# Optimization experiments

Hardware: AMD Instinct MI355X
Metric: run time of the kernel (lower is better)

The kernel has to match this reference:

```python
import jax, jax.numpy as jnp
import numpy as np

N, E, D, H, O = 50000, 600000, 128, 128, 64


def _glorot(key, shape):
    fan_in, fan_out = shape[-1], shape[0]
    lim = (6.0 / (fan_in + fan_out)) ** 0.5
    return jax.random.uniform(key, shape, jnp.float32, -lim, lim)


def setup_inputs() -> dict:
    key = jax.random.key(0)
    ks = jax.random.split(key, 20)
    inp = {
        'x': jax.random.normal(ks[0], (N, D), dtype=jnp.float32),
        'edge_index': jax.random.randint(ks[1], (2, E), 0, N, dtype=jnp.int32),
        # FastLocalConv params
        'fl_W': _glorot(ks[2], (H, D)),
        'fl_b': jnp.zeros((H,), jnp.float32),
        'fl_att': _glorot(ks[3], (1, H)),
        # GIN layer 1 MLP: Linear(H,H) -> ReLU -> Linear(H,H)
        'g1_W1': _glorot(ks[4], (H, H)), 'g1_b1': jnp.zeros((H,), jnp.float32),
        'g1_W2': _glorot(ks[5], (H, H)), 'g1_b2': jnp.zeros((H,), jnp.float32),
        # GIN layer 2 MLP
        'g2_W1': _glorot(ks[6], (H, H)), 'g2_b1': jnp.zeros((H,), jnp.float32),
        'g2_W2': _glorot(ks[7], (H, H)), 'g2_b2': jnp.zeros((H,), jnp.float32),
        # output head
        'out_W': _glorot(ks[8], (O, H)), 'out_b': jnp.zeros((O,), jnp.float32),
    }
    return inp


def _fast_local(x, edge_index, W, b, att):
    # add self loops
    loops = jnp.arange(N, dtype=edge_index.dtype)
    row = jnp.concatenate([edge_index[0], loops])
    col = jnp.concatenate([edge_index[1], loops])
    h = x @ W.T + b                                   # [N,H]
    alpha = jax.nn.leaky_relu((h[row] * att[0]).sum(-1), 0.2)  # [E+N]
    # scatter-softmax grouped by source node (row), as in original code
    m = jax.ops.segment_max(alpha, row, num_segments=N)
    ea = jnp.exp(alpha - m[row])
    s = jax.ops.segment_sum(ea, row, num_segments=N)
    a = ea / s[row]
    # aggr='add' into target nodes (col), message = alpha * x_j (x_j = h[row])
    return jax.ops.segment_sum(a[:, None] * h[row], col, num_segments=N)


def _gin(h, edge_index, W1, b1, W2, b2):
    # GINConv (eps=0): mlp(x + sum_{j in N(i)} x_j), no self loops
    agg = jax.ops.segment_sum(h[edge_index[0]], edge_index[1], num_segments=N)
    z = h + agg
    z = jax.nn.relu(z @ W1.T + b1)
    return z @ W2.T + b2


def reference(x, edge_index, fl_W, fl_b, fl_att,
              g1_W1, g1_b1, g1_W2, g1_b2,
              g2_W1, g2_b1, g2_W2, g2_b2,
              out_W, out_b):
    h = _fast_local(x, edge_index, fl_W, fl_b, fl_att)
    h = jax.nn.relu(h)  # (dropout is eval no-op)
    h = jax.nn.relu(_gin(h, edge_index, g1_W1, g1_b1, g1_W2, g1_b2))
    h = jax.nn.relu(_gin(h, edge_index, g2_W1, g2_b1, g2_W2, g2_b2))
    logits = h @ out_W.T + out_b
    return jax.nn.log_softmax(logits, axis=1)
```

## Files before the change

### kernel.cpp

```cpp
#include <hip/hip_runtime.h>
#include <stdint.h>

typedef __attribute__((ext_vector_type(8))) short short8;
typedef __attribute__((ext_vector_type(4))) float floatx4;

#define HB 64
#define HW 12500

__device__ inline unsigned short f2bf(float f) {
  union { float f; unsigned int u; } v; v.f = f;
  unsigned int u = v.u;
  unsigned int r = (u + 0x7FFFu + ((u >> 16) & 1u)) >> 16;
  return (unsigned short)r;
}
__device__ inline unsigned int pk2(float a, float b) {
  return (unsigned int)f2bf(a) | ((unsigned int)f2bf(b) << 16);
}
__device__ inline void acc8(uint4 u, float* a) {
  a[0] += __uint_as_float(u.x << 16); a[1] += __uint_as_float(u.x & 0xffff0000u);
  a[2] += __uint_as_float(u.y << 16); a[3] += __uint_as_float(u.y & 0xffff0000u);
  a[4] += __uint_as_float(u.z << 16); a[5] += __uint_as_float(u.z & 0xffff0000u);
  a[6] += __uint_as_float(u.w << 16); a[7] += __uint_as_float(u.w & 0xffff0000u);
}
__device__ inline uint4 pk8(const float* a) {
  uint4 p;
  p.x = pk2(a[0], a[1]); p.y = pk2(a[2], a[3]);
  p.z = pk2(a[4], a[5]); p.w = pk2(a[6], a[7]);
  return p;
}

__global__ __launch_bounds__(256) void k_wconv(const float* __restrict__ s0, const float* __restrict__ s1,
                                               const float* __restrict__ s2, const float* __restrict__ s3,
                                               const float* __restrict__ s4, const float* __restrict__ s5,
                                               unsigned short* __restrict__ dst) {
  int b = blockIdx.x;
  int seg = b >> 4;
  int rel = b & 15;
  const float* sp[6] = {s0, s1, s2, s3, s4, s5};
  const float* src = sp[seg];
  int i = rel * 1024 + threadIdx.x * 4;
  float4 v = *(const float4*)(src + i);
  size_t o = (size_t)seg * 16384 + i;
  *(uint2*)(dst + o) = make_uint2(pk2(v.x, v.y), pk2(v.z, v.w));
}

__global__ __launch_bounds__(1024) void k_hist(const int* __restrict__ esrc,
                                               const int* __restrict__ edst,
                                               int E, int per,
                                               unsigned int* __restrict__ pAll) {
  __shared__ unsigned int h[HW];
  for (int i = threadIdx.x; i < HW; i += 1024) h[i] = 0;
  __syncthreads();
  const int* idx = blockIdx.y ? esrc : edst;
  int s = blockIdx.x * per, e = min(E, s + per);
  for (int j = s + threadIdx.x; j < e; j += 1024) {
    unsigned int d = (unsigned int)idx[j];
    atomicAdd(&h[d >> 2], 1u << ((d & 3) * 8));
  }
  __syncthreads();
  unsigned int* p = pAll + ((size_t)blockIdx.y * HB + blockIdx.x) * HW;
  for (int i = threadIdx.x; i < HW; i += 1024) p[i] = h[i];
}

__global__ __launch_bounds__(256) void k_reduce(unsigned int* __restrict__ pAll,
                                                int* __restrict__ deg,
                                                float* __restrict__ invc, int N) {
  int w = blockIdx.x * 256 + threadIdx.x;
  if (w >= HW) return;
  unsigned int* pd = pAll + w;
  const unsigned int* ps = pAll + (size_t)HB * HW + w;
  unsigned int r0 = 0, r1 = 0, r2 = 0, r3 = 0;
  for (int b = 0; b < HB; ++b) {
    unsigned int v = pd[(size_t)b * HW];
    pd[(size_t)b * HW] = r0 | (r1 << 8) | (r2 << 16) | (r3 << 24);
    r0 += v & 255u; r1 += (v >> 8) & 255u; r2 += (v >> 16) & 255u; r3 += v >> 24;
  }
  unsigned int s0 = 0, s1 = 0, s2 = 0, s3 = 0;
  for (int b = 0; b < HB; ++b) {
    unsigned int v = ps[(size_t)b * HW];
    s0 += v & 255u; s1 += (v >> 8) & 255u; s2 += (v >> 16) & 255u; s3 += v >> 24;
  }
  int n0 = 4 * w;
  unsigned int rr[4] = {r0, r1, r2, r3}, ss[4] = {s0, s1, s2, s3};
#pragma unroll
  for (int c = 0; c < 4; ++c) {
    if (n0 + c < N) {
      deg[n0 + c] = (int)rr[c];
      invc[n0 + c] = 1.0f / (1.0f + (float)ss[c]);
    }
  }
}

__global__ __launch_bounds__(1024) void k_scan_local(const int* __restrict__ deg,
                                                     int* __restrict__ off,
                                                     int* __restrict__ bsum, int N) {
  __shared__ int sb[1024];
  int tid = threadIdx.x;
  int i = blockIdx.x * 1024 + tid;
  int v = (i < N) ? deg[i] : 0;
  sb[tid] = v;
  __syncthreads();
  for (int d = 1; d < 1024; d <<= 1) {
    int t = (tid >= d) ? sb[tid - d] : 0;
    __syncthreads();
    sb[tid] += t;
    __syncthreads();
  }
  if (i < N) off[i] = sb[tid] - v;
  if (tid == 1023) bsum[blockIdx.x] = sb[1023];
}

__global__ __launch_bounds__(256) void k_scan_fix(int* off, const int* __restrict__ bsum,
                                                  int N, int E) {
  int i = blockIdx.x * 256 + threadIdx.x;
  if (i >= N) return;
  int nb = i >> 10;
  int s = 0;
  for (int c = 0; c < nb; ++c) s += bsum[c];
  off[i] += s;
  if (i == 0) off[N] = E;
}

__global__ __launch_bounds__(1024) void k_fill2(const int* __restrict__ esrc,
                                                const int* __restrict__ edst,
                                                int E, int per,
                                                const unsigned int* __restrict__ pAll,
                                                const int* __restrict__ off,
                                                int* __restrict__ srcs) {
  __shared__ unsigned int rk[HW];
  for (int i = threadIdx.x; i < HW; i += 1024) rk[i] = 0;
  __syncthreads();
  const unsigned int* slab = pAll + (size_t)blockIdx.x * HW;
  int s = blockIdx.x * per, e = min(E, s + per);
  for (int j = s + threadIdx.x; j < e; j += 1024) {
    unsigned int d = (unsigned int)edst[j];
    int sh = (d & 3) * 8;
    unsigned int rank = (atomicAdd(&rk[d >> 2], 1u << sh) >> sh) & 255u;
    unsigned int base = (slab[d >> 2] >> sh) & 255u;
    srcs[off[d] + (int)base + (int)rank] = esrc[j];
  }
}

__global__ __launch_bounds__(256) void k_gemm_fl(const float* __restrict__ in,
                                                 const unsigned short* __restrict__ Wb,
                                                 const float* __restrict__ bias,
                                                 const float* __restrict__ scale,
                                                 unsigned short* __restrict__ out, int N) {
  __shared__ unsigned short sx[64 * 136];
  __shared__ unsigned short sw[128 * 136];
  const int tid = threadIdx.x;
  const int nb = blockIdx.x * 64;

  for (int i = tid; i < 128 * 16; i += 256) {
    int h = i >> 4, c = i & 15;
    *(short8*)&sw[h * 136 + c * 8] = ((const short8*)Wb)[i];
  }
  for (int i = tid; i < 64 * 32; i += 256) {
    int n = i >> 5, k4 = i & 31;
    int gn = nb + n;
    float4 xv;
    if (gn < N) xv = ((const float4*)in)[(size_t)gn * 32 + k4];
    else { xv.x = 0.f; xv.y = 0.f; xv.z = 0.f; xv.w = 0.f; }
    *(uint2*)&sx[n * 136 + k4 * 4] = make_uint2(pk2(xv.x, xv.y), pk2(xv.z, xv.w));
  }
  __syncthreads();

  const int wave = tid >> 6, lane = tid & 63;
  const int quad = lane >> 4, lq = lane & 15;
  floatx4 acc[8];
#pragma unroll
  for (int t = 0; t < 8; ++t) acc[t] = (floatx4){0.f, 0.f, 0.f, 0.f};
  const int arow = (wave * 16 + lq) * 136;
#pragma unroll
  for (int kt = 0; kt < 4; ++kt) {
    short8 a = *(const short8*)&sx[arow + kt * 32 + quad * 8];
#pragma unroll
    for (int t = 0; t < 8; ++t) {
      short8 b = *(const short8*)&sw[(t * 16 + lq) * 136 + kt * 32 + quad * 8];
      acc[t] = __builtin_amdgcn_mfma_f32_16x16x32_bf16(a, b, acc[t], 0, 0, 0);
    }
  }
#pragma unroll
  for (int t = 0; t < 8; ++t) {
    int h = t * 16 + lq;
    float bv = bias[h];
#pragma unroll
    for (int r = 0; r < 4; ++r) {
      int n = nb + wave * 16 + quad * 4 + r;
      if (n < N) out[(size_t)n * 128 + h] = f2bf((acc[t][r] + bv) * scale[n]);
    }
  }
}

template <bool RELU_OUT>
__global__ __launch_bounds__(256) void k_agg(const uint4* __restrict__ G,
                                             uint4* __restrict__ out,
                                             const int* __restrict__ off,
                                             const int* __restrict__ srcs, int N) {
  int n = (blockIdx.x * 256 + threadIdx.x) >> 4;
  if (n >= N) return;
  int l = threadIdx.x & 15;
  float a[8] = {0, 0, 0, 0, 0, 0, 0, 0};
  acc8(G[(size_t)n * 16 + l], a);
  int s = off[n], e = off[n + 1];
  int j = s;
  for (; j + 8 <= e; j += 8) {
    int i0 = srcs[j],     i1 = srcs[j + 1], i2 = srcs[j + 2], i3 = srcs[j + 3];
    int i4 = srcs[j + 4], i5 = srcs[j + 5], i6 = srcs[j + 6], i7 = srcs[j + 7];
    uint4 u0 = G[(size_t)i0 * 16 + l];
    uint4 u1 = G[(size_t)i1 * 16 + l];
    uint4 u2 = G[(size_t)i2 * 16 + l];
    uint4 u3 = G[(size_t)i3 * 16 + l];
    uint4 u4 = G[(size_t)i4 * 16 + l];
    uint4 u5 = G[(size_t)i5 * 16 + l];
    uint4 u6 = G[(size_t)i6 * 16 + l];
    uint4 u7 = G[(size_t)i7 * 16 + l];
    acc8(u0, a); acc8(u1, a); acc8(u2, a); acc8(u3, a);
    acc8(u4, a); acc8(u5, a); acc8(u6, a); acc8(u7, a);
  }
  if (j + 4 <= e) {
    int i0 = srcs[j], i1 = srcs[j + 1], i2 = srcs[j + 2], i3 = srcs[j + 3];
    uint4 u0 = G[(size_t)i0 * 16 + l];
    uint4 u1 = G[(size_t)i1 * 16 + l];
    uint4 u2 = G[(size_t)i2 * 16 + l];
    uint4 u3 = G[(size_t)i3 * 16 + l];
    acc8(u0, a); acc8(u1, a); acc8(u2, a); acc8(u3, a);
    j += 4;
  }
  for (; j < e; ++j) acc8(G[(size_t)srcs[j] * 16 + l], a);
  if (RELU_OUT) {
#pragma unroll
    for (int q = 0; q < 8; ++q) a[q] = fmaxf(a[q], 0.f);
  }
  out[(size_t)n * 16 + l] = pk8(a);
}

__global__ __launch_bounds__(256) void k_mlp(const unsigned short* __restrict__ in,
                                             const unsigned short* __restrict__ W1b,
                                             const float* __restrict__ b1,
                                             const unsigned short* __restrict__ W2b,
                                             const float* __restrict__ b2,
                                             unsigned short* __restrict__ out, int N) {
  __shared__ unsigned short sx[64 * 136];
  __shared__ unsigned short sw[128 * 136];
  const int tid = threadIdx.x;
  const int nb = blockIdx.x * 64;

  for (int i = tid; i < 128 * 16; i += 256) {
    int h = i >> 4, c = i & 15;
    *(short8*)&sw[h * 136 + c * 8] = ((const short8*)W1b)[i];
  }
  for (int i = tid; i < 64 * 16; i += 256) {
    int n = i >> 4, c = i & 15;
    int gn = nb + n;
    short8 t;
    if (gn < N) t = *(const short8*)(in + (size_t)gn * 128 + c * 8);
    else t = (short8){0, 0, 0, 0, 0, 0, 0, 0};
    *(short8*)&sx[n * 136 + c * 8] = t;
  }
  __syncthreads();

  const int wave = tid >> 6, lane = tid & 63;
  const int quad = lane >> 4, lq = lane & 15;
  const int arow = (wave * 16 + lq) * 136;

  floatx4 acc[8];
#pragma unroll
  for (int t = 0; t < 8; ++t) acc[t] = (floatx4){0.f, 0.f, 0.f, 0.f};
#pragma unroll
  for (int kt = 0; kt < 4; ++kt) {
    short8 a = *(const short8*)&sx[arow + kt * 32 + quad * 8];
#pragma unroll
    for (int t = 0; t < 8; ++t) {
      short8 b = *(const short8*)&sw[(t * 16 + lq) * 136 + kt * 32 + quad * 8];
      acc[t] = __builtin_amdgcn_mfma_f32_16x16x32_bf16(a, b, acc[t], 0, 0, 0);
    }
  }
  __syncthreads();

#pragma unroll
  for (int t = 0; t < 8; ++t) {
    int h = t * 16 + lq;
    float bv = b1[h];
#pragma unroll
    for (int r = 0; r < 4; ++r) {
      int row = wave * 16 + quad * 4 + r;
      sx[row * 136 + h] = f2bf(fmaxf(acc[t][r] + bv, 0.f));
    }
  }
  for (int i = tid; i < 128 * 16; i += 256) {
    int h = i >> 4, c = i & 15;
    *(short8*)&sw[h * 136 + c * 8] = ((const short8*)W2b)[i];
  }
  __syncthreads();

#pragma unroll
  for (int t = 0; t < 8; ++t) acc[t] = (floatx4){0.f, 0.f, 0.f, 0.f};
#pragma unroll
  for (int kt = 0; kt < 4; ++kt) {
    short8 a = *(const short8*)&sx[arow + kt * 32 + quad * 8];
#pragma unroll
    for (int t = 0; t < 8; ++t) {
      short8 b = *(const short8*)&sw[(t * 16 + lq) * 136 + kt * 32 + quad * 8];
      acc[t] = __builtin_amdgcn_mfma_f32_16x16x32_bf16(a, b, acc[t], 0, 0, 0);
    }
  }
#pragma unroll
  for (int t = 0; t < 8; ++t) {
    int h = t * 16 + lq;
    float bv = b2[h];
#pragma unroll
    for (int r = 0; r < 4; ++r) {
      int n = nb + wave * 16 + quad * 4 + r;
      if (n < N) out[(size_t)n * 128 + h] = f2bf(fmaxf(acc[t][r] + bv, 0.f));
    }
  }
}

__global__ __launch_bounds__(256) void k_head(const unsigned short* __restrict__ in,
                                              const unsigned short* __restrict__ Wb,
                                              const float* __restrict__ bias,
                                              float* __restrict__ out, int N) {
  __shared__ unsigned short sx[64 * 136];
  __shared__ unsigned short sw[64 * 136];
  const int tid = threadIdx.x;
  const int nb = blockIdx.x * 64;

  for (int i = tid; i < 64 * 16; i += 256) {
    int h = i >> 4, c = i & 15;
    *(short8*)&sw[h * 136 + c * 8] = ((const short8*)Wb)[i];
  }
  for (int i = tid; i < 64 * 16; i += 256) {
    int n = i >> 4, c = i & 15;
    int gn = nb + n;
    short8 t;
    if (gn < N) t = *(const short8*)(in + (size_t)gn * 128 + c * 8);
    else t = (short8){0, 0, 0, 0, 0, 0, 0, 0};
    *(short8*)&sx[n * 136 + c * 8] = t;
  }
  __syncthreads();

  const int wave = tid >> 6, lane = tid & 63;
  const int quad = lane >> 4, lq = lane & 15;
  floatx4 acc[4];
#pragma unroll
  for (int t = 0; t < 4; ++t) acc[t] = (floatx4){0.f, 0.f, 0.f, 0.f};
  const int arow = (wave * 16 + lq) * 136;
#pragma unroll
  for (int kt = 0; kt < 4; ++kt) {
    short8 a = *(const short8*)&sx[arow + kt * 32 + quad * 8];
#pragma unroll
    for (int t = 0; t < 4; ++t) {
      short8 b = *(const short8*)&sw[(t * 16 + lq) * 136 + kt * 32 + quad * 8];
      acc[t] = __builtin_amdgcn_mfma_f32_16x16x32_bf16(a, b, acc[t], 0, 0, 0);
    }
  }
  float v[4][4];
#pragma unroll
  for (int t = 0; t < 4; ++t) {
    float bv = bias[t * 16 + lq];
#pragma unroll
    for (int r = 0; r < 4; ++r) v[t][r] = acc[t][r] + bv;
  }
#pragma unroll
  for (int r = 0; r < 4; ++r) {
    float m = fmaxf(fmaxf(v[0][r], v[1][r]), fmaxf(v[2][r], v[3][r]));
    m = fmaxf(m, __shfl_xor(m, 1));
    m = fmaxf(m, __shfl_xor(m, 2));
    m = fmaxf(m, __shfl_xor(m, 4));
    m = fmaxf(m, __shfl_xor(m, 8));
    float s = expf(v[0][r] - m) + expf(v[1][r] - m) + expf(v[2][r] - m) + expf(v[3][r] - m);
    s += __shfl_xor(s, 1);
    s += __shfl_xor(s, 2);
    s += __shfl_xor(s, 4);
    s += __shfl_xor(s, 8);
    float l = m + logf(s);
    int n = nb + wave * 16 + quad * 4 + r;
    if (n < N) {
#pragma unroll
      for (int t = 0; t < 4; ++t) out[(size_t)n * 64 + t * 16 + lq] = v[t][r] - l;
    }
  }
}

extern "C" void kernel_launch(void* const* d_in, const int* in_sizes, int n_in,
                              void* d_out, int out_size, void* d_ws, size_t ws_size,
                              hipStream_t stream) {
  const float* x     = (const float*)d_in[0];
  const int*   edges = (const int*)  d_in[1];
  const float* fl_W  = (const float*)d_in[2];
  const float* fl_b  = (const float*)d_in[3];
  const float* g1_W1 = (const float*)d_in[5];
  const float* g1_b1 = (const float*)d_in[6];
  const float* g1_W2 = (const float*)d_in[7];
  const float* g1_b2 = (const float*)d_in[8];
  const float* g2_W1 = (const float*)d_in[9];
  const float* g2_b1 = (const float*)d_in[10];
  const float* g2_W2 = (const float*)d_in[11];
  const float* g2_b2 = (const float*)d_in[12];
  const float* out_W = (const float*)d_in[13];
  const float* out_b = (const float*)d_in[14];

  const int N = in_sizes[0] / 128;
  const int E = in_sizes[1] / 2;
  const int* esrc = edges;
  const int* edst = edges + E;

  char* w = (char*)d_ws;
  unsigned short* A = (unsigned short*)w;  w += (size_t)N * 128 * 2;
  unsigned short* B = (unsigned short*)w;  w += (size_t)N * 128 * 2;
  unsigned short* C = (unsigned short*)w;  w += (size_t)N * 128 * 2;
  unsigned short* Wb = (unsigned short*)w; w += 90112 * 2;
  int* deg    = (int*)w;   w += (size_t)N * 4;
  int* off    = (int*)w;   w += (size_t)(N + 1) * 4;
  float* invc = (float*)w; w += (size_t)N * 4;
  int* bsum   = (int*)w;   w += 1024 * 4;
  int* srcs   = (int*)w;   w += (size_t)E * 4;
  unsigned int* pAll = (unsigned int*)w; w += (size_t)2 * HB * HW * 4;

  const int GB = (N + 63) / 64;
  const int AGB = (N * 16 + 255) / 256;
  const int nchunk = (N + 1023) / 1024;
  const int per = (E + HB - 1) / HB;

  k_wconv<<<88, 256, 0, stream>>>(fl_W, g1_W1, g1_W2, g2_W1, g2_W2, out_W, Wb);

  k_hist<<<dim3(HB, 2), 1024, 0, stream>>>(esrc, edst, E, per, pAll);
  k_reduce<<<(HW + 255) / 256, 256, 0, stream>>>(pAll, deg, invc, N);
  k_scan_local<<<nchunk, 1024, 0, stream>>>(deg, off, bsum, N);
  k_scan_fix<<<(N + 255) / 256, 256, 0, stream>>>(off, bsum, N, E);
  k_fill2<<<HB, 1024, 0, stream>>>(esrc, edst, E, per, pAll, off, srcs);

  k_gemm_fl<<<GB, 256, 0, stream>>>(x, Wb, fl_b, invc, A, N);
  k_agg<true><<<AGB, 256, 0, stream>>>((const uint4*)A, (uint4*)B, off, srcs, N);

  k_agg<false><<<AGB, 256, 0, stream>>>((const uint4*)B, (uint4*)C, off, srcs, N);
  k_mlp<<<GB, 256, 0, stream>>>(C, Wb + 16384, g1_b1, Wb + 32768, g1_b2, A, N);

  k_agg<false><<<AGB, 256, 0, stream>>>((const uint4*)A, (uint4*)C, off, srcs, N);
  k_mlp<<<GB, 256, 0, stream>>>(C, Wb + 49152, g2_b1, Wb + 65536, g2_b2, B, N);

  k_head<<<GB, 256, 0, stream>>>(B, Wb + 81920, out_b, (float*)d_out, N);
}
```

Before: 295.8 us.

## Fuse degree reduction with local prefix scan and vectorize shared-memory clears

Merges the histogram reduction kernel and the local scan kernel into one kernel. Each thread handles four packed node counters and scans their sum, which removes the intermediate degree array and one launch. Each scan block now covers 4096 nodes, and the offsets are written as int4. Shared histogram zeroing and the copy-out now use uint4 accesses. The trade-off is that the fused kernel runs with only 13 blocks of 1024 threads, so the strided 64-slab reduction loop has little parallelism.

```diff
diff --git a/kernel.cpp b/kernel.cpp
--- a/kernel.cpp
+++ b/kernel.cpp
@@ -48,8 +48,9 @@
                                                const int* __restrict__ edst,
                                                int E, int per,
                                                unsigned int* __restrict__ pAll) {
-  __shared__ unsigned int h[HW];
-  for (int i = threadIdx.x; i < HW; i += 1024) h[i] = 0;
+  __shared__ __align__(16) unsigned int h[HW];
+  uint4* h4 = (uint4*)h;
+  for (int i = threadIdx.x; i < HW / 4; i += 1024) h4[i] = make_uint4(0, 0, 0, 0);
   __syncthreads();
   const int* idx = blockIdx.y ? esrc : edst;
   int s = blockIdx.x * per, e = min(E, s + per);
@@ -58,47 +59,45 @@
     atomicAdd(&h[d >> 2], 1u << ((d & 3) * 8));
   }
   __syncthreads();
-  unsigned int* p = pAll + ((size_t)blockIdx.y * HB + blockIdx.x) * HW;
-  for (int i = threadIdx.x; i < HW; i += 1024) p[i] = h[i];
-}
-
-__global__ __launch_bounds__(256) void k_reduce(unsigned int* __restrict__ pAll,
-                                                int* __restrict__ deg,
-                                                float* __restrict__ invc, int N) {
-  int w = blockIdx.x * 256 + threadIdx.x;
-  if (w >= HW) return;
-  unsigned int* pd = pAll + w;
-  const unsigned int* ps = pAll + (size_t)HB * HW + w;
-  unsigned int r0 = 0, r1 = 0, r2 = 0, r3 = 0;
-  for (int b = 0; b < HB; ++b) {
-    unsigned int v = pd[(size_t)b * HW];
-    pd[(size_t)b * HW] = r0 | (r1 << 8) | (r2 << 16) | (r3 << 24);
-    r0 += v & 255u; r1 += (v >> 8) & 255u; r2 += (v >> 16) & 255u; r3 += v >> 24;
-  }
-  unsigned int s0 = 0, s1 = 0, s2 = 0, s3 = 0;
-  for (int b = 0; b < HB; ++b) {
-    unsigned int v = ps[(size_t)b * HW];
-    s0 += v & 255u; s1 += (v >> 8) & 255u; s2 += (v >> 16) & 255u; s3 += v >> 24;
-  }
-  int n0 = 4 * w;
-  unsigned int rr[4] = {r0, r1, r2, r3}, ss[4] = {s0, s1, s2, s3};
-#pragma unroll
-  for (int c = 0; c < 4; ++c) {
-    if (n0 + c < N) {
-      deg[n0 + c] = (int)rr[c];
-      invc[n0 + c] = 1.0f / (1.0f + (float)ss[c]);
-    }
-  }
-}
-
-__global__ __launch_bounds__(1024) void k_scan_local(const int* __restrict__ deg,
-                                                     int* __restrict__ off,
-                                                     int* __restrict__ bsum, int N) {
+  uint4* p4 = (uint4*)(pAll + ((size_t)blockIdx.y * HB + blockIdx.x) * HW);
+  for (int i = threadIdx.x; i < HW / 4; i += 1024) p4[i] = h4[i];
+}
+
+__global__ __launch_bounds__(1024) void k_degscan(unsigned int* __restrict__ pAll,
+                                                  int* __restrict__ off,
+                                                  float* __restrict__ invc,
+                                                  int* __restrict__ bsum, int N) {
   __shared__ int sb[1024];
   int tid = threadIdx.x;
-  int i = blockIdx.x * 1024 + tid;
-  int v = (i < N) ? deg[i] : 0;
-  sb[tid] = v;
+  int w = blockIdx.x * 1024 + tid;
+  unsigned int r0 = 0, r1 = 0, r2 = 0, r3 = 0;
+  if (w < HW) {
+    unsigned int* pd = pAll + w;
+    for (int b = 0; b < HB; ++b) {
+      unsigned int v = pd[(size_t)b * HW];
+      pd[(size_t)b * HW] = r0 | (r1 << 8) | (r2 << 16) | (r3 << 24);
+      r0 += v & 255u; r1 += (v >> 8) & 255u; r2 += (v >> 16) & 255u; r3 += v >> 24;
+    }
+    const unsigned int* ps = pAll + (size_t)HB * HW + w;
+    unsigned int s0 = 0, s1 = 0, s2 = 0, s3 = 0;
+    for (int b = 0; b < HB; ++b) {
+      unsigned int v = ps[(size_t)b * HW];
+      s0 += v & 255u; s1 += (v >> 8) & 255u; s2 += (v >> 16) & 255u; s3 += v >> 24;
+    }
+    int n0 = 4 * w;
+    float i0 = 1.0f / (1.0f + (float)s0), i1 = 1.0f / (1.0f + (float)s1);
+    float i2 = 1.0f / (1.0f + (float)s2), i3 = 1.0f / (1.0f + (float)s3);
+    if (n0 + 3 < N) {
+      invc[n0] = i0; invc[n0 + 1] = i1; invc[n0 + 2] = i2; invc[n0 + 3] = i3;
+    } else {
+      if (n0 < N) invc[n0] = i0;
+      if (n0 + 1 < N) invc[n0 + 1] = i1;
+      if (n0 + 2 < N) invc[n0 + 2] = i2;
+      if (n0 + 3 < N) invc[n0 + 3] = i3;
+    }
+  }
+  int L = (w < HW) ? (int)(r0 + r1 + r2 + r3) : 0;
+  sb[tid] = L;
   __syncthreads();
   for (int d = 1; d < 1024; d <<= 1) {
     int t = (tid >= d) ? sb[tid - d] : 0;
@@ -106,7 +105,15 @@
     sb[tid] += t;
     __syncthreads();
   }
-  if (i < N) off[i] = sb[tid] - v;
+  int base = sb[tid] - L;
+  if (w < HW) {
+    int4 o;
+    o.x = base;
+    o.y = o.x + (int)r0;
+    o.z = o.y + (int)r1;
+    o.w = o.z + (int)r2;
+    *(int4*)(off + 4 * w) = o;
+  }
   if (tid == 1023) bsum[blockIdx.x] = sb[1023];
 }
 
@@ -114,7 +121,7 @@
                                                   int N, int E) {
   int i = blockIdx.x * 256 + threadIdx.x;
   if (i >= N) return;
-  int nb = i >> 10;
+  int nb = i >> 12;
   int s = 0;
   for (int c = 0; c < nb; ++c) s += bsum[c];
   off[i] += s;
@@ -127,8 +134,9 @@
                                                 const unsigned int* __restrict__ pAll,
                                                 const int* __restrict__ off,
                                                 int* __restrict__ srcs) {
-  __shared__ unsigned int rk[HW];
-  for (int i = threadIdx.x; i < HW; i += 1024) rk[i] = 0;
+  __shared__ __align__(16) unsigned int rk[HW];
+  uint4* rk4 = (uint4*)rk;
+  for (int i = threadIdx.x; i < HW / 4; i += 1024) rk4[i] = make_uint4(0, 0, 0, 0);
   __syncthreads();
   const unsigned int* slab = pAll + (size_t)blockIdx.x * HW;
   int s = blockIdx.x * per, e = min(E, s + per);
@@ -411,23 +419,20 @@
   unsigned short* B = (unsigned short*)w;  w += (size_t)N * 128 * 2;
   unsigned short* C = (unsigned short*)w;  w += (size_t)N * 128 * 2;
   unsigned short* Wb = (unsigned short*)w; w += 90112 * 2;
-  int* deg    = (int*)w;   w += (size_t)N * 4;
-  int* off    = (int*)w;   w += (size_t)(N + 1) * 4;
+  int* off    = (int*)w;   w += (size_t)(4 * HW + 16) * 4;
   float* invc = (float*)w; w += (size_t)N * 4;
-  int* bsum   = (int*)w;   w += 1024 * 4;
+  int* bsum   = (int*)w;   w += 64 * 4;
   int* srcs   = (int*)w;   w += (size_t)E * 4;
   unsigned int* pAll = (unsigned int*)w; w += (size_t)2 * HB * HW * 4;
 
   const int GB = (N + 63) / 64;
   const int AGB = (N * 16 + 255) / 256;
-  const int nchunk = (N + 1023) / 1024;
   const int per = (E + HB - 1) / HB;
 
   k_wconv<<<88, 256, 0, stream>>>(fl_W, g1_W1, g1_W2, g2_W1, g2_W2, out_W, Wb);
 
   k_hist<<<dim3(HB, 2), 1024, 0, stream>>>(esrc, edst, E, per, pAll);
-  k_reduce<<<(HW + 255) / 256, 256, 0, stream>>>(pAll, deg, invc, N);
-  k_scan_local<<<nchunk, 1024, 0, stream>>>(deg, off, bsum, N);
+  k_degscan<<<(HW + 1023) / 1024, 1024, 0, stream>>>(pAll, off, invc, bsum, N);
   k_scan_fix<<<(N + 255) / 256, 256, 0, stream>>>(off, bsum, N, E);
   k_fill2<<<HB, 1024, 0, stream>>>(esrc, edst, E, per, pAll, off, srcs);
 
```

Result: no change. 299.5 us (+1.3%).
